# Optimization experiments

Hardware: AMD Instinct MI355X
Metric: run time of the kernel (lower is better)

The kernel has to match this reference:

```python
import jax, jax.numpy as jnp
import numpy as np

B, N, PHY, C, HID, FC, L, E = 2, 8192, 2, 64, 64, 128, 3, 524288

def _ln(x, g, b, eps=1e-5):
    mu = jnp.mean(x, axis=-1, keepdims=True)
    var = jnp.mean((x - mu) ** 2, axis=-1, keepdims=True)
    return (x - mu) * jax.lax.rsqrt(var + eps) * g + b

def setup_inputs() -> dict:
    key = jax.random.key(0)
    ks = jax.random.split(key, 24)
    s = 1.0 / np.sqrt(C)
    inp = {
        'x': jax.random.normal(ks[0], (B, N, 5), jnp.float32),
        'edge_index': jax.random.randint(ks[1], (2, E), 0, B * N, jnp.int32),
        'fc0_w': jax.random.normal(ks[2], (C, 4), jnp.float32) * 0.5,
        'fc0_b': jnp.zeros((C,), jnp.float32),
        'ln0_g': jnp.ones((C,), jnp.float32),
        'ln0_b': jnp.zeros((C,), jnp.float32),
        'gg_fc1_w': jax.random.normal(ks[3], (L, HID, C), jnp.float32) * s,
        'gg_fc1_b': jnp.zeros((L, HID), jnp.float32),
        'gg_fc2_w': jax.random.normal(ks[4], (L, C, HID), jnp.float32) * s,
        'gg_fc2_b': jnp.zeros((L, C), jnp.float32),
        'gg_weight': jax.random.uniform(ks[5], (L, HID), jnp.float32) + 0.5,
        'gg_freq': jax.random.normal(ks[6], (L, PHY, HID), jnp.float32) * (2 * np.pi),
        'wc_w': jax.random.normal(ks[7], (L, C, C), jnp.float32) * s,
        'wc_b': jnp.zeros((L, C), jnp.float32),
        'ln_g': jnp.ones((L, C), jnp.float32),
        'ln_b': jnp.zeros((L, C), jnp.float32),
        'fc1_w': jax.random.normal(ks[8], (FC, C), jnp.float32) * s,
        'fc1_b': jnp.zeros((FC,), jnp.float32),
        'fc2_w': jax.random.normal(ks[9], (1, FC), jnp.float32) / np.sqrt(FC),
        'fc2_b': jnp.zeros((1,), jnp.float32),
    }
    return inp

def reference(x, edge_index, fc0_w, fc0_b, ln0_g, ln0_b, gg_fc1_w, gg_fc1_b,
              gg_fc2_w, gg_fc2_b, gg_weight, gg_freq, wc_w, wc_b, ln_g, ln_b,
              fc1_w, fc1_b, fc2_w, fc2_b):
    grid = x[:, :, 2:4]           # (B,N,PHY): columns in_dim-phy_dim .. -1
    gw = x[:, :, 4]               # (B,N) grid_weight
    feat = x[:, :, :4]            # (B,N,in_dim)
    src, dst = edge_index[0], edge_index[1]
    grid_f = grid.reshape(-1, PHY)
    gw_f = gw.reshape(-1)
    vec = grid_f[src] - grid_f[dst]                      # (E,PHY)
    dist2 = jnp.sum(vec * vec, axis=-1, keepdims=True)   # (E,1)
    wgt_src = gw_f[src][:, None]                          # (E,1)

    h = feat @ fc0_w.T + fc0_b                            # (B,N,C)
    h = _ln(h, ln0_g, ln0_b)
    for l in range(L):
        w = gg_weight[l]                                  # (HID,)
        gauss = jnp.sqrt((w / jnp.pi) ** PHY) * jnp.exp(-w * dist2)  # (E,HID)
        fourier = jnp.sin(vec @ gg_freq[l])               # (E,HID)
        morlet = gauss * fourier
        hl = h @ gg_fc1_w[l].T + gg_fc1_b[l]              # (B,N,HID)
        val = morlet * hl.reshape(-1, HID)[src] * wgt_src # (E,HID)
        agg = jax.ops.segment_sum(val, dst, num_segments=B * N)
        x1 = agg.reshape(B, N, HID) @ gg_fc2_w[l].T + gg_fc2_b[l]
        x2 = h @ wc_w[l].T + wc_b[l]                      # pointwise Conv1d
        h = _ln(x1 + x2, ln_g[l], ln_b[l])
        if l != L - 1:
            h = jax.nn.gelu(h, approximate=False)
    h = jax.nn.gelu(h @ fc1_w.T + fc1_b, approximate=False)
    return h @ fc2_w.T + fc2_b                            # (B,N,1)
```

## Files before the change

### kernel.cpp

```cpp
#include <hip/hip_runtime.h>
#include <hip/hip_bf16.h>

#define M_NODES 16384
#define E_EDGES 524288
#define ASTR 68

typedef short short8 __attribute__((ext_vector_type(8)));
typedef float f32x4 __attribute__((ext_vector_type(4)));
typedef unsigned int uint4v __attribute__((ext_vector_type(4)));

static __device__ __forceinline__ float wredsum(float v) {
#pragma unroll
  for (int o = 32; o > 0; o >>= 1) v += __shfl_xor(v, o, 64);
  return v;
}

static __device__ __forceinline__ float gelu_exact(float x) {
  return 0.5f * x * (1.0f + erff(x * 0.70710678118654752440f));
}

static __device__ __forceinline__ unsigned int bsplit(float x) {
  unsigned int u = __float_as_uint(x);
  unsigned int hb = (u + 0x7FFFu + ((u >> 16) & 1u)) >> 16;
  float hf = __uint_as_float(hb << 16);
  float r = x - hf;
  unsigned int v = __float_as_uint(r);
  unsigned int lb = (v + 0x7FFFu + ((v >> 16) & 1u)) >> 16;
  return (hb & 0xFFFFu) | (lb << 16);
}

struct Frag { short8 hi, lo; };

static __device__ __forceinline__ Frag load_afrag(const unsigned int* a) {
  uint4v u0 = *(const uint4v*)a;
  uint4v u1 = *(const uint4v*)(a + 4);
  Frag f;
#pragma unroll
  for (int j = 0; j < 4; ++j) {
    f.hi[j]     = (short)(u0[j] & 0xFFFFu);
    f.lo[j]     = (short)(u0[j] >> 16);
    f.hi[j + 4] = (short)(u1[j] & 0xFFFFu);
    f.lo[j + 4] = (short)(u1[j] >> 16);
  }
  return f;
}

static __device__ __forceinline__ Frag load_bfrag(const float* __restrict__ w) {
  float4 w0 = *(const float4*)w;
  float4 w1 = *(const float4*)(w + 4);
  float v[8] = {w0.x, w0.y, w0.z, w0.w, w1.x, w1.y, w1.z, w1.w};
  Frag f;
#pragma unroll
  for (int j = 0; j < 8; ++j) {
    unsigned int p = bsplit(v[j]);
    f.hi[j] = (short)(p & 0xFFFFu);
    f.lo[j] = (short)(p >> 16);
  }
  return f;
}

static __device__ __forceinline__ f32x4 mfma3(const Frag& a, const Frag& b, f32x4 c) {
  c = __builtin_amdgcn_mfma_f32_16x16x32_bf16(a.hi, b.hi, c, 0, 0, 0);
  c = __builtin_amdgcn_mfma_f32_16x16x32_bf16(a.lo, b.hi, c, 0, 0, 0);
  c = __builtin_amdgcn_mfma_f32_16x16x32_bf16(a.hi, b.lo, c, 0, 0, 0);
  return c;
}

static __device__ __forceinline__ void gemm64(const unsigned int* Arow,
                                              const float* __restrict__ W,
                                              int c, int q, f32x4 acc[4]) {
  Frag a0 = load_afrag(Arow + 8 * q);
  Frag a1 = load_afrag(Arow + 32 + 8 * q);
#pragma unroll
  for (int t = 0; t < 4; ++t) {
    Frag b0 = load_bfrag(W + (16 * t + c) * 64 + 8 * q);
    Frag b1 = load_bfrag(W + (16 * t + c) * 64 + 32 + 8 * q);
    acc[t] = mfma3(a0, b0, acc[t]);
    acc[t] = mfma3(a1, b1, acc[t]);
  }
}

static __device__ __forceinline__ void store_d(float* __restrict__ O,
                                               const float* __restrict__ bias,
                                               int tilebase, int c, int q,
                                               const f32x4 acc[4]) {
#pragma unroll
  for (int t = 0; t < 4; ++t) {
    float bn = bias[16 * t + c];
#pragma unroll
    for (int r = 0; r < 4; ++r)
      O[(tilebase + 4 * q + r) * 64 + 16 * t + c] = acc[t][r] + bn;
  }
}

__global__ __launch_bounds__(256) void k_init(
    const float* __restrict__ x,
    const float* __restrict__ fc0_w, const float* __restrict__ fc0_b,
    const float* __restrict__ ln0_g, const float* __restrict__ ln0_b,
    const float* __restrict__ w1, const float* __restrict__ b1,
    const float* __restrict__ wc, const float* __restrict__ wcb,
    float2* __restrict__ grid2, float* __restrict__ gwf,
    float* __restrict__ hl, float* __restrict__ x2)
{
  __shared__ unsigned int A[64 * ASTR];
  const int tid = threadIdx.x;
  const int lane = tid & 63;
  const int w = tid >> 6;
  const int tilebase = blockIdx.x * 64 + w * 16;

  float fw0 = fc0_w[lane * 4 + 0], fw1 = fc0_w[lane * 4 + 1];
  float fw2v = fc0_w[lane * 4 + 2], fw3 = fc0_w[lane * 4 + 3];
  float fb = fc0_b[lane], g0 = ln0_g[lane], bb0 = ln0_b[lane];

  for (int i = 0; i < 16; ++i) {
    int node = tilebase + i;
    float xv0 = x[node * 5 + 0], xv1 = x[node * 5 + 1], xv2 = x[node * 5 + 2];
    float xv3 = x[node * 5 + 3], xv4 = x[node * 5 + 4];
    float acc = fb + xv0 * fw0 + xv1 * fw1 + xv2 * fw2v + xv3 * fw3;
    float mean = wredsum(acc) * (1.0f / 64.0f);
    float d = acc - mean;
    float var = wredsum(d * d) * (1.0f / 64.0f);
    float hv = d * rsqrtf(var + 1e-5f) * g0 + bb0;
    A[(w * 16 + i) * ASTR + lane] = bsplit(hv);
    if (lane == 0) { grid2[node] = make_float2(xv2, xv3); gwf[node] = xv4; }
  }
  __syncthreads();

  const int c = lane & 15, q = lane >> 4;
  const unsigned int* Arow = A + (w * 16 + c) * ASTR;

  f32x4 z = {0.f, 0.f, 0.f, 0.f};
  f32x4 acc1[4] = {z, z, z, z};
  gemm64(Arow, w1, c, q, acc1);
  store_d(hl, b1, tilebase, c, q, acc1);

  f32x4 acc2[4] = {z, z, z, z};
  gemm64(Arow, wc, c, q, acc2);
  store_d(x2, wcb, tilebase, c, q, acc2);
}

__global__ __launch_bounds__(256) void k_count(const int* __restrict__ ei, int* __restrict__ cnt)
{
  int e = blockIdx.x * 256 + threadIdx.x;
  if (e < E_EDGES) atomicAdd(&cnt[ei[E_EDGES + e]], 1);
}

__global__ __launch_bounds__(1024) void k_scan(const int* __restrict__ cnt,
                                               int* __restrict__ row_start,
                                               int* __restrict__ cursor)
{
  const int PER = M_NODES / 1024;
  const int t = threadIdx.x;
  const int base = t * PER;
  int local[PER];
  int s = 0;
#pragma unroll
  for (int k = 0; k < PER; ++k) { local[k] = cnt[base + k]; s += local[k]; }

  __shared__ int part[1024];
  part[t] = s;
  __syncthreads();
  for (int off = 1; off < 1024; off <<= 1) {
    int v = (t >= off) ? part[t - off] : 0;
    __syncthreads();
    part[t] += v;
    __syncthreads();
  }
  int run = part[t] - s;
#pragma unroll
  for (int k = 0; k < PER; ++k) {
    row_start[base + k] = run;
    cursor[base + k] = run;
    run += local[k];
  }
  if (t == 1023) row_start[M_NODES] = run;
}

__global__ __launch_bounds__(256) void k_scatter(
    const int* __restrict__ ei, const float2* __restrict__ grid2,
    const float* __restrict__ gwf, int* __restrict__ cursor,
    float4* __restrict__ rec)
{
  int e = blockIdx.x * 256 + threadIdx.x;
  if (e < E_EDGES) {
    int s = ei[e];
    int dd = ei[E_EDGES + e];
    int pos = atomicAdd(&cursor[dd], 1);
    float2 gs = grid2[s], gd = grid2[dd];
    rec[pos] = make_float4(gs.x - gd.x, gs.y - gd.y, gwf[s], __int_as_float(s));
  }
}

__global__ __launch_bounds__(256) void k_agg(
    const float4* __restrict__ rec, const int* __restrict__ row_start,
    const float* __restrict__ hl,
    const float* __restrict__ gw, const float* __restrict__ freq,
    float* __restrict__ agg)
{
  const int lane = threadIdx.x & 63;
  const int node = blockIdx.x * 4 + (threadIdx.x >> 6);

  const float w = gw[lane];
  const float nwl2 = -w * 1.44269504088896340736f;
  const float lc = log2f(w * 0.31830988618379067154f);
  const float f0s = freq[lane] * 0.15915494309189533577f;
  const float f1s = freq[64 + lane] * 0.15915494309189533577f;

  const int beg = row_start[node];
  const int end = row_start[node + 1];
  float acc = 0.0f;

  int i = beg;
  if (i < end) {
    float4 r = rec[i];
    float hlv = hl[__float_as_int(r.w) * 64 + lane];
    for (++i; i < end; ++i) {
      float4 rn = rec[i];
      float hn = hl[__float_as_int(rn.w) * 64 + lane];
      float dist2 = r.x * r.x + r.y * r.y;
      float gs = __builtin_amdgcn_exp2f(__builtin_fmaf(nwl2, dist2, lc));
      float rev = __builtin_fmaf(r.x, f0s, r.y * f1s);
      float fo = __builtin_amdgcn_sinf(__builtin_amdgcn_fractf(rev));
      acc = __builtin_fmaf(gs * fo * hlv, r.z, acc);
      r = rn; hlv = hn;
    }
    float dist2 = r.x * r.x + r.y * r.y;
    float gs = __builtin_amdgcn_exp2f(__builtin_fmaf(nwl2, dist2, lc));
    float rev = __builtin_fmaf(r.x, f0s, r.y * f1s);
    float fo = __builtin_amdgcn_sinf(__builtin_amdgcn_fractf(rev));
    acc = __builtin_fmaf(gs * fo * hlv, r.z, acc);
  }
  agg[node * 64 + lane] = acc;
}

__global__ __launch_bounds__(256) void k_post_mid(
    const float* __restrict__ agg,
    const float* __restrict__ w2, const float* __restrict__ b2,
    const float* __restrict__ lng, const float* __restrict__ lnb,
    const float* __restrict__ nw1, const float* __restrict__ nb1,
    const float* __restrict__ nwc, const float* __restrict__ nwcb,
    float* __restrict__ hl, float* __restrict__ x2)
{
  __shared__ unsigned int A[64 * ASTR];
  const int tid = threadIdx.x, lane = tid & 63, w = tid >> 6;
  const int tilebase = blockIdx.x * 64 + w * 16;
  const int c = lane & 15, q = lane >> 4;

  float x2v[4][4], lg[4], lb[4], vb[4];
#pragma unroll
  for (int t = 0; t < 4; ++t) {
    int n = 16 * t + c;
    lg[t] = lng[n]; lb[t] = lnb[n]; vb[t] = b2[n];
#pragma unroll
    for (int r = 0; r < 4; ++r)
      x2v[t][r] = x2[(tilebase + 4 * q + r) * 64 + n];
  }

  {
    int rr = lane >> 2, cc = (lane & 3) * 16;
    const float* src = agg + (tilebase + rr) * 64 + cc;
    unsigned int* dstp = A + (16 * w + rr) * ASTR + cc;
#pragma unroll
    for (int j4 = 0; j4 < 4; ++j4) {
      float4 v = *(const float4*)(src + 4 * j4);
      uint4v pv;
      pv[0] = bsplit(v.x); pv[1] = bsplit(v.y); pv[2] = bsplit(v.z); pv[3] = bsplit(v.w);
      *(uint4v*)(dstp + 4 * j4) = pv;
    }
  }
  __syncthreads();

  const unsigned int* Arow = A + (16 * w + c) * ASTR;
  f32x4 z = {0.f, 0.f, 0.f, 0.f};
  f32x4 acc[4] = {z, z, z, z};
  gemm64(Arow, w2, c, q, acc);

  float v[4][4];
#pragma unroll
  for (int t = 0; t < 4; ++t)
#pragma unroll
    for (int r = 0; r < 4; ++r)
      v[t][r] = acc[t][r] + vb[t] + x2v[t][r];

  float mean[4], var[4];
#pragma unroll
  for (int r = 0; r < 4; ++r) {
    float s = v[0][r] + v[1][r] + v[2][r] + v[3][r];
    s += __shfl_xor(s, 1, 64); s += __shfl_xor(s, 2, 64);
    s += __shfl_xor(s, 4, 64); s += __shfl_xor(s, 8, 64);
    mean[r] = s * (1.0f / 64.0f);
  }
#pragma unroll
  for (int r = 0; r < 4; ++r) {
    float s = 0.f;
#pragma unroll
    for (int t = 0; t < 4; ++t) { float d = v[t][r] - mean[r]; s += d * d; }
    s += __shfl_xor(s, 1, 64); s += __shfl_xor(s, 2, 64);
    s += __shfl_xor(s, 4, 64); s += __shfl_xor(s, 8, 64);
    var[r] = s * (1.0f / 64.0f);
  }
#pragma unroll
  for (int t = 0; t < 4; ++t)
#pragma unroll
    for (int r = 0; r < 4; ++r) {
      float d = v[t][r] - mean[r];
      float h = d * rsqrtf(var[r] + 1e-5f) * lg[t] + lb[t];
      v[t][r] = gelu_exact(h);
    }

#pragma unroll
  for (int t = 0; t < 4; ++t)
#pragma unroll
    for (int r = 0; r < 4; ++r)
      A[(16 * w + 4 * q + r) * ASTR + 16 * t + c] = bsplit(v[t][r]);

  f32x4 acch[4] = {z, z, z, z};
  gemm64(Arow, nw1, c, q, acch);
  store_d(hl, nb1, tilebase, c, q, acch);

  f32x4 accx[4] = {z, z, z, z};
  gemm64(Arow, nwc, c, q, accx);
  store_d(x2, nwcb, tilebase, c, q, accx);
}

__global__ __launch_bounds__(256) void k_post_last(
    const float* __restrict__ agg,
    const float* __restrict__ w2, const float* __restrict__ b2,
    const float* __restrict__ lng, const float* __restrict__ lnb,
    const float* __restrict__ x2,
    const float* __restrict__ fc1w, const float* __restrict__ fc1b,
    const float* __restrict__ fw2, const float* __restrict__ fb2,
    float* __restrict__ out)
{
  __shared__ unsigned int A[64 * ASTR];
  const int tid = threadIdx.x, lane = tid & 63, w = tid >> 6;
  const int tilebase = blockIdx.x * 64 + w * 16;
  const int c = lane & 15, q = lane >> 4;

  float x2v[4][4], lg[4], lb[4], vb[4];
#pragma unroll
  for (int t = 0; t < 4; ++t) {
    int n = 16 * t + c;
    lg[t] = lng[n]; lb[t] = lnb[n]; vb[t] = b2[n];
#pragma unroll
    for (int r = 0; r < 4; ++r)
      x2v[t][r] = x2[(tilebase + 4 * q + r) * 64 + n];
  }

  {
    int rr = lane >> 2, cc = (lane & 3) * 16;
    const float* src = agg + (tilebase + rr) * 64 + cc;
    unsigned int* dstp = A + (16 * w + rr) * ASTR + cc;
#pragma unroll
    for (int j4 = 0; j4 < 4; ++j4) {
      float4 v = *(const float4*)(src + 4 * j4);
      uint4v pv;
      pv[0] = bsplit(v.x); pv[1] = bsplit(v.y); pv[2] = bsplit(v.z); pv[3] = bsplit(v.w);
      *(uint4v*)(dstp + 4 * j4) = pv;
    }
  }
  __syncthreads();

  const unsigned int* Arow = A + (16 * w + c) * ASTR;
  f32x4 z = {0.f, 0.f, 0.f, 0.f};
  f32x4 acc[4] = {z, z, z, z};
  gemm64(Arow, w2, c, q, acc);

  float v[4][4];
#pragma unroll
  for (int t = 0; t < 4; ++t)
#pragma unroll
    for (int r = 0; r < 4; ++r)
      v[t][r] = acc[t][r] + vb[t] + x2v[t][r];

  float mean[4], var[4];
#pragma unroll
  for (int r = 0; r < 4; ++r) {
    float s = v[0][r] + v[1][r] + v[2][r] + v[3][r];
    s += __shfl_xor(s, 1, 64); s += __shfl_xor(s, 2, 64);
    s += __shfl_xor(s, 4, 64); s += __shfl_xor(s, 8, 64);
    mean[r] = s * (1.0f / 64.0f);
  }
#pragma unroll
  for (int r = 0; r < 4; ++r) {
    float s = 0.f;
#pragma unroll
    for (int t = 0; t < 4; ++t) { float d = v[t][r] - mean[r]; s += d * d; }
    s += __shfl_xor(s, 1, 64); s += __shfl_xor(s, 2, 64);
    s += __shfl_xor(s, 4, 64); s += __shfl_xor(s, 8, 64);
    var[r] = s * (1.0f / 64.0f);
  }
#pragma unroll
  for (int t = 0; t < 4; ++t)
#pragma unroll
    for (int r = 0; r < 4; ++r) {
      float d = v[t][r] - mean[r];
      v[t][r] = d * rsqrtf(var[r] + 1e-5f) * lg[t] + lb[t];
    }

#pragma unroll
  for (int t = 0; t < 4; ++t)
#pragma unroll
    for (int r = 0; r < 4; ++r)
      A[(16 * w + 4 * q + r) * ASTR + 16 * t + c] = bsplit(v[t][r]);

  Frag a0 = load_afrag(Arow + 8 * q);
  Frag a1 = load_afrag(Arow + 32 + 8 * q);
  float p[4] = {0.f, 0.f, 0.f, 0.f};
#pragma unroll
  for (int t8 = 0; t8 < 8; ++t8) {
    Frag b0 = load_bfrag(fc1w + (16 * t8 + c) * 64 + 8 * q);
    Frag b1 = load_bfrag(fc1w + (16 * t8 + c) * 64 + 32 + 8 * q);
    f32x4 a = z;
    a = mfma3(a0, b0, a);
    a = mfma3(a1, b1, a);
    float fbv = fc1b[16 * t8 + c];
    float fwv = fw2[16 * t8 + c];
#pragma unroll
    for (int r = 0; r < 4; ++r) p[r] += gelu_exact(a[r] + fbv) * fwv;
  }
#pragma unroll
  for (int r = 0; r < 4; ++r) {
    float s = p[r];
    s += __shfl_xor(s, 1, 64); s += __shfl_xor(s, 2, 64);
    s += __shfl_xor(s, 4, 64); s += __shfl_xor(s, 8, 64);
    p[r] = s;
  }
  if (c == 0) {
    float bb = fb2[0];
#pragma unroll
    for (int r = 0; r < 4; ++r) out[tilebase + 4 * q + r] = p[r] + bb;
  }
}

extern "C" void kernel_launch(void* const* d_in, const int* in_sizes, int n_in,
                              void* d_out, int out_size, void* d_ws, size_t ws_size,
                              hipStream_t stream) {
  const float* x     = (const float*)d_in[0];
  const int* ei      = (const int*)d_in[1];
  const float* fc0_w = (const float*)d_in[2];
  const float* fc0_b = (const float*)d_in[3];
  const float* ln0_g = (const float*)d_in[4];
  const float* ln0_b = (const float*)d_in[5];
  const float* gg_fc1_w = (const float*)d_in[6];
  const float* gg_fc1_b = (const float*)d_in[7];
  const float* gg_fc2_w = (const float*)d_in[8];
  const float* gg_fc2_b = (const float*)d_in[9];
  const float* gg_weight = (const float*)d_in[10];
  const float* gg_freq   = (const float*)d_in[11];
  const float* wc_w = (const float*)d_in[12];
  const float* wc_b = (const float*)d_in[13];
  const float* ln_g = (const float*)d_in[14];
  const float* ln_b = (const float*)d_in[15];
  const float* fc1_w = (const float*)d_in[16];
  const float* fc1_b = (const float*)d_in[17];
  const float* fc2_w = (const float*)d_in[18];
  const float* fc2_b = (const float*)d_in[19];

  char* ws = (char*)d_ws;
  size_t off = 0;
  auto alloc = [&](size_t bytes) -> void* {
    void* p = ws + off;
    off = (off + bytes + 255) & ~(size_t)255;
    return p;
  };
  float2* grid2   = (float2*)alloc((size_t)M_NODES * 8);
  float*  gwf     = (float*)alloc((size_t)M_NODES * 4);
  float*  hl      = (float*)alloc((size_t)M_NODES * 64 * 4);
  float*  agg     = (float*)alloc((size_t)M_NODES * 64 * 4);
  float*  x2      = (float*)alloc((size_t)M_NODES * 64 * 4);
  int*    cnt     = (int*)alloc((size_t)M_NODES * 4);
  int*    cursor  = (int*)alloc((size_t)M_NODES * 4);
  int*    row_st  = (int*)alloc((size_t)(M_NODES + 1) * 4);
  float4* rec     = (float4*)alloc((size_t)E_EDGES * 16);
  (void)ws_size; (void)in_sizes; (void)n_in; (void)out_size;

  hipMemsetAsync(cnt, 0, (size_t)M_NODES * 4, stream);

  k_init<<<M_NODES / 64, 256, 0, stream>>>(x, fc0_w, fc0_b, ln0_g, ln0_b,
                                           gg_fc1_w, gg_fc1_b, wc_w, wc_b,
                                           grid2, gwf, hl, x2);
  k_count<<<E_EDGES / 256, 256, 0, stream>>>(ei, cnt);
  k_scan<<<1, 1024, 0, stream>>>(cnt, row_st, cursor);
  k_scatter<<<E_EDGES / 256, 256, 0, stream>>>(ei, grid2, gwf, cursor, rec);

  for (int l = 0; l < 3; ++l) {
    k_agg<<<M_NODES / 4, 256, 0, stream>>>(rec, row_st, hl,
                                           gg_weight + l * 64, gg_freq + l * 128, agg);
    if (l < 2) {
      k_post_mid<<<M_NODES / 64, 256, 0, stream>>>(
          agg,
          gg_fc2_w + l * 4096, gg_fc2_b + l * 64,
          ln_g + l * 64, ln_b + l * 64,
          gg_fc1_w + (l + 1) * 4096, gg_fc1_b + (l + 1) * 64,
          wc_w + (l + 1) * 4096, wc_b + (l + 1) * 64,
          hl, x2);
    } else {
      k_post_last<<<M_NODES / 64, 256, 0, stream>>>(
          agg,
          gg_fc2_w + l * 4096, gg_fc2_b + l * 64,
          ln_g + l * 64, ln_b + l * 64,
          x2,
          fc1_w, fc1_b, fc2_w, fc2_b,
          (float*)d_out);
    }
  }
}
```

Before: 310.3 us.

## Split dense node GEMMs across waves by output column, 16 nodes per block

The node-wise dense kernels (init, post_mid, post_last) now process 16 nodes per block instead of 64. Each of the four waves computes a 16-column slice of the output rather than all 64 columns for its own 16 rows. Grids grow from 256 to 1024 blocks, which gives more parallelism across CUs and fewer registers per thread. The cost is that LayerNorm statistics need a cross-wave reduction through shared memory with extra barriers, and variance now uses the single-pass E[x^2]-mean^2 form, which is slightly less numerically stable.

Result: faster. 288.0 us (-7.2%).

```diff
diff --git a/kernel.cpp b/kernel.cpp
--- a/kernel.cpp
+++ b/kernel.cpp
@@ -66,31 +66,17 @@
   return c;
 }
 
-static __device__ __forceinline__ void gemm64(const unsigned int* Arow,
-                                              const float* __restrict__ W,
-                                              int c, int q, f32x4 acc[4]) {
-  Frag a0 = load_afrag(Arow + 8 * q);
-  Frag a1 = load_afrag(Arow + 32 + 8 * q);
-#pragma unroll
-  for (int t = 0; t < 4; ++t) {
-    Frag b0 = load_bfrag(W + (16 * t + c) * 64 + 8 * q);
-    Frag b1 = load_bfrag(W + (16 * t + c) * 64 + 32 + 8 * q);
-    acc[t] = mfma3(a0, b0, acc[t]);
-    acc[t] = mfma3(a1, b1, acc[t]);
-  }
-}
-
-static __device__ __forceinline__ void store_d(float* __restrict__ O,
-                                               const float* __restrict__ bias,
-                                               int tilebase, int c, int q,
-                                               const f32x4 acc[4]) {
-#pragma unroll
-  for (int t = 0; t < 4; ++t) {
-    float bn = bias[16 * t + c];
-#pragma unroll
-    for (int r = 0; r < 4; ++r)
-      O[(tilebase + 4 * q + r) * 64 + 16 * t + c] = acc[t][r] + bn;
-  }
+static __device__ __forceinline__ f32x4 gemm16(const unsigned int* __restrict__ A,
+                                               const float* __restrict__ W,
+                                               int n, int c, int q) {
+  Frag a0 = load_afrag(A + c * ASTR + 8 * q);
+  Frag a1 = load_afrag(A + c * ASTR + 32 + 8 * q);
+  Frag b0 = load_bfrag(W + n * 64 + 8 * q);
+  Frag b1 = load_bfrag(W + n * 64 + 32 + 8 * q);
+  f32x4 acc = {0.f, 0.f, 0.f, 0.f};
+  acc = mfma3(a0, b0, acc);
+  acc = mfma3(a1, b1, acc);
+  return acc;
 }
 
 __global__ __launch_bounds__(256) void k_init(
@@ -102,18 +88,17 @@
     float2* __restrict__ grid2, float* __restrict__ gwf,
     float* __restrict__ hl, float* __restrict__ x2)
 {
-  __shared__ unsigned int A[64 * ASTR];
-  const int tid = threadIdx.x;
-  const int lane = tid & 63;
-  const int w = tid >> 6;
-  const int tilebase = blockIdx.x * 64 + w * 16;
+  __shared__ unsigned int A[16 * ASTR];
+  const int tid = threadIdx.x, lane = tid & 63, w = tid >> 6;
+  const int tilebase = blockIdx.x * 16;
 
   float fw0 = fc0_w[lane * 4 + 0], fw1 = fc0_w[lane * 4 + 1];
   float fw2v = fc0_w[lane * 4 + 2], fw3 = fc0_w[lane * 4 + 3];
   float fb = fc0_b[lane], g0 = ln0_g[lane], bb0 = ln0_b[lane];
 
-  for (int i = 0; i < 16; ++i) {
-    int node = tilebase + i;
+#pragma unroll
+  for (int i = 0; i < 4; ++i) {
+    int node = tilebase + 4 * w + i;
     float xv0 = x[node * 5 + 0], xv1 = x[node * 5 + 1], xv2 = x[node * 5 + 2];
     float xv3 = x[node * 5 + 3], xv4 = x[node * 5 + 4];
     float acc = fb + xv0 * fw0 + xv1 * fw1 + xv2 * fw2v + xv3 * fw3;
@@ -121,22 +106,25 @@
     float d = acc - mean;
     float var = wredsum(d * d) * (1.0f / 64.0f);
     float hv = d * rsqrtf(var + 1e-5f) * g0 + bb0;
-    A[(w * 16 + i) * ASTR + lane] = bsplit(hv);
+    A[(4 * w + i) * ASTR + lane] = bsplit(hv);
     if (lane == 0) { grid2[node] = make_float2(xv2, xv3); gwf[node] = xv4; }
   }
   __syncthreads();
 
   const int c = lane & 15, q = lane >> 4;
-  const unsigned int* Arow = A + (w * 16 + c) * ASTR;
-
-  f32x4 z = {0.f, 0.f, 0.f, 0.f};
-  f32x4 acc1[4] = {z, z, z, z};
-  gemm64(Arow, w1, c, q, acc1);
-  store_d(hl, b1, tilebase, c, q, acc1);
-
-  f32x4 acc2[4] = {z, z, z, z};
-  gemm64(Arow, wc, c, q, acc2);
-  store_d(x2, wcb, tilebase, c, q, acc2);
+  const int n = 16 * w + c;
+
+  f32x4 a1v = gemm16(A, w1, n, c, q);
+  float b1v = b1[n];
+#pragma unroll
+  for (int r = 0; r < 4; ++r)
+    hl[(tilebase + 4 * q + r) * 64 + n] = a1v[r] + b1v;
+
+  f32x4 a2v = gemm16(A, wc, n, c, q);
+  float wcbv = wcb[n];
+#pragma unroll
+  for (int r = 0; r < 4; ++r)
+    x2[(tilebase + 4 * q + r) * 64 + n] = a2v[r] + wcbv;
 }
 
 __global__ __launch_bounds__(256) void k_count(const int* __restrict__ ei, int* __restrict__ cnt)
@@ -241,86 +229,71 @@
     const float* __restrict__ nwc, const float* __restrict__ nwcb,
     float* __restrict__ hl, float* __restrict__ x2)
 {
-  __shared__ unsigned int A[64 * ASTR];
+  __shared__ unsigned int A[16 * ASTR];
+  __shared__ float PS[4][16], PQ[4][16];
   const int tid = threadIdx.x, lane = tid & 63, w = tid >> 6;
-  const int tilebase = blockIdx.x * 64 + w * 16;
+  const int tilebase = blockIdx.x * 16;
   const int c = lane & 15, q = lane >> 4;
-
-  float x2v[4][4], lg[4], lb[4], vb[4];
-#pragma unroll
-  for (int t = 0; t < 4; ++t) {
-    int n = 16 * t + c;
-    lg[t] = lng[n]; lb[t] = lnb[n]; vb[t] = b2[n];
-#pragma unroll
-    for (int r = 0; r < 4; ++r)
-      x2v[t][r] = x2[(tilebase + 4 * q + r) * 64 + n];
-  }
+  const int n = 16 * w + c;
+
+  float x2v[4];
+#pragma unroll
+  for (int r = 0; r < 4; ++r)
+    x2v[r] = x2[(tilebase + 4 * q + r) * 64 + n];
+  float lg = lng[n], lb = lnb[n], vb = b2[n];
 
   {
-    int rr = lane >> 2, cc = (lane & 3) * 16;
-    const float* src = agg + (tilebase + rr) * 64 + cc;
-    unsigned int* dstp = A + (16 * w + rr) * ASTR + cc;
-#pragma unroll
-    for (int j4 = 0; j4 < 4; ++j4) {
-      float4 v = *(const float4*)(src + 4 * j4);
-      uint4v pv;
-      pv[0] = bsplit(v.x); pv[1] = bsplit(v.y); pv[2] = bsplit(v.z); pv[3] = bsplit(v.w);
-      *(uint4v*)(dstp + 4 * j4) = pv;
+    int i = tid * 4;
+    int row = i >> 6, col = i & 63;
+    float4 v = *(const float4*)(agg + tilebase * 64 + i);
+    uint4v pv;
+    pv[0] = bsplit(v.x); pv[1] = bsplit(v.y); pv[2] = bsplit(v.z); pv[3] = bsplit(v.w);
+    *(uint4v*)(A + row * ASTR + col) = pv;
+  }
+  __syncthreads();
+
+  f32x4 acc = gemm16(A, w2, n, c, q);
+
+  float S[4];
+#pragma unroll
+  for (int r = 0; r < 4; ++r) S[r] = acc[r] + vb + x2v[r];
+
+#pragma unroll
+  for (int r = 0; r < 4; ++r) {
+    float s1 = S[r], s2 = S[r] * S[r];
+#pragma unroll
+    for (int m = 1; m < 16; m <<= 1) {
+      s1 += __shfl_xor(s1, m, 64);
+      s2 += __shfl_xor(s2, m, 64);
     }
-  }
-  __syncthreads();
-
-  const unsigned int* Arow = A + (16 * w + c) * ASTR;
-  f32x4 z = {0.f, 0.f, 0.f, 0.f};
-  f32x4 acc[4] = {z, z, z, z};
-  gemm64(Arow, w2, c, q, acc);
-
-  float v[4][4];
-#pragma unroll
-  for (int t = 0; t < 4; ++t)
-#pragma unroll
-    for (int r = 0; r < 4; ++r)
-      v[t][r] = acc[t][r] + vb[t] + x2v[t][r];
-
-  float mean[4], var[4];
+    if (c == 0) { PS[w][4 * q + r] = s1; PQ[w][4 * q + r] = s2; }
+  }
+  __syncthreads();
+
 #pragma unroll
   for (int r = 0; r < 4; ++r) {
-    float s = v[0][r] + v[1][r] + v[2][r] + v[3][r];
-    s += __shfl_xor(s, 1, 64); s += __shfl_xor(s, 2, 64);
-    s += __shfl_xor(s, 4, 64); s += __shfl_xor(s, 8, 64);
-    mean[r] = s * (1.0f / 64.0f);
-  }
-#pragma unroll
-  for (int r = 0; r < 4; ++r) {
-    float s = 0.f;
-#pragma unroll
-    for (int t = 0; t < 4; ++t) { float d = v[t][r] - mean[r]; s += d * d; }
-    s += __shfl_xor(s, 1, 64); s += __shfl_xor(s, 2, 64);
-    s += __shfl_xor(s, 4, 64); s += __shfl_xor(s, 8, 64);
-    var[r] = s * (1.0f / 64.0f);
-  }
-#pragma unroll
-  for (int t = 0; t < 4; ++t)
-#pragma unroll
-    for (int r = 0; r < 4; ++r) {
-      float d = v[t][r] - mean[r];
-      float h = d * rsqrtf(var[r] + 1e-5f) * lg[t] + lb[t];
-      v[t][r] = gelu_exact(h);
-    }
-
-#pragma unroll
-  for (int t = 0; t < 4; ++t)
-#pragma unroll
-    for (int r = 0; r < 4; ++r)
-      A[(16 * w + 4 * q + r) * ASTR + 16 * t + c] = bsplit(v[t][r]);
-
-  f32x4 acch[4] = {z, z, z, z};
-  gemm64(Arow, nw1, c, q, acch);
-  store_d(hl, nb1, tilebase, c, q, acch);
-
-  f32x4 accx[4] = {z, z, z, z};
-  gemm64(Arow, nwc, c, q, accx);
-  store_d(x2, nwcb, tilebase, c, q, accx);
+    int row = 4 * q + r;
+    float sum = PS[0][row] + PS[1][row] + PS[2][row] + PS[3][row];
+    float sq  = PQ[0][row] + PQ[1][row] + PQ[2][row] + PQ[3][row];
+    float mean = sum * (1.0f / 64.0f);
+    float var = sq * (1.0f / 64.0f) - mean * mean;
+    float hv = (S[r] - mean) * rsqrtf(var + 1e-5f) * lg + lb;
+    hv = gelu_exact(hv);
+    A[row * ASTR + n] = bsplit(hv);
+  }
+  __syncthreads();
+
+  f32x4 a1v = gemm16(A, nw1, n, c, q);
+  float b1v = nb1[n];
+#pragma unroll
+  for (int r = 0; r < 4; ++r)
+    hl[(tilebase + 4 * q + r) * 64 + n] = a1v[r] + b1v;
+
+  f32x4 a2v = gemm16(A, nwc, n, c, q);
+  float wcbv = nwcb[n];
+#pragma unroll
+  for (int r = 0; r < 4; ++r)
+    x2[(tilebase + 4 * q + r) * 64 + n] = a2v[r] + wcbv;
 }
 
 __global__ __launch_bounds__(256) void k_post_last(
@@ -332,105 +305,84 @@
     const float* __restrict__ fw2, const float* __restrict__ fb2,
     float* __restrict__ out)
 {
-  __shared__ unsigned int A[64 * ASTR];
+  __shared__ unsigned int A[16 * ASTR];
+  __shared__ float PS[4][16], PQ[4][16];
   const int tid = threadIdx.x, lane = tid & 63, w = tid >> 6;
-  const int tilebase = blockIdx.x * 64 + w * 16;
+  const int tilebase = blockIdx.x * 16;
   const int c = lane & 15, q = lane >> 4;
-
-  float x2v[4][4], lg[4], lb[4], vb[4];
-#pragma unroll
-  for (int t = 0; t < 4; ++t) {
-    int n = 16 * t + c;
-    lg[t] = lng[n]; lb[t] = lnb[n]; vb[t] = b2[n];
-#pragma unroll
-    for (int r = 0; r < 4; ++r)
-      x2v[t][r] = x2[(tilebase + 4 * q + r) * 64 + n];
-  }
+  const int n = 16 * w + c;
+
+  float x2v[4];
+#pragma unroll
+  for (int r = 0; r < 4; ++r)
+    x2v[r] = x2[(tilebase + 4 * q + r) * 64 + n];
+  float lg = lng[n], lb = lnb[n], vb = b2[n];
 
   {
-    int rr = lane >> 2, cc = (lane & 3) * 16;
-    const float* src = agg + (tilebase + rr) * 64 + cc;
-    unsigned int* dstp = A + (16 * w + rr) * ASTR + cc;
-#pragma unroll
-    for (int j4 = 0; j4 < 4; ++j4) {
-      float4 v = *(const float4*)(src + 4 * j4);
-      uint4v pv;
-      pv[0] = bsplit(v.x); pv[1] = bsplit(v.y); pv[2] = bsplit(v.z); pv[3] = bsplit(v.w);
-      *(uint4v*)(dstp + 4 * j4) = pv;
+    int i = tid * 4;
+    int row = i >> 6, col = i & 63;
+    float4 v = *(const float4*)(agg + tilebase * 64 + i);
+    uint4v pv;
+    pv[0] = bsplit(v.x); pv[1] = bsplit(v.y); pv[2] = bsplit(v.z); pv[3] = bsplit(v.w);
+    *(uint4v*)(A + row * ASTR + col) = pv;
+  }
+  __syncthreads();
+
+  f32x4 acc = gemm16(A, w2, n, c, q);
+
+  float S[4];
+#pragma unroll
+  for (int r = 0; r < 4; ++r) S[r] = acc[r] + vb + x2v[r];
+
+#pragma unroll
+  for (int r = 0; r < 4; ++r) {
+    float s1 = S[r], s2 = S[r] * S[r];
+#pragma unroll
+    for (int m = 1; m < 16; m <<= 1) {
+      s1 += __shfl_xor(s1, m, 64);
+      s2 += __shfl_xor(s2, m, 64);
     }
-  }
-  __syncthreads();
-
-  const unsigned int* Arow = A + (16 * w + c) * ASTR;
-  f32x4 z = {0.f, 0.f, 0.f, 0.f};
-  f32x4 acc[4] = {z, z, z, z};
-  gemm64(Arow, w2, c, q, acc);
-
-  float v[4][4];
-#pragma unroll
-  for (int t = 0; t < 4; ++t)
-#pragma unroll
-    for (int r = 0; r < 4; ++r)
-      v[t][r] = acc[t][r] + vb[t] + x2v[t][r];
-
-  float mean[4], var[4];
+    if (c == 0) { PS[w][4 * q + r] = s1; PQ[w][4 * q + r] = s2; }
+  }
+  __syncthreads();
+
 #pragma unroll
   for (int r = 0; r < 4; ++r) {
-    float s = v[0][r] + v[1][r] + v[2][r] + v[3][r];
-    s += __shfl_xor(s, 1, 64); s += __shfl_xor(s, 2, 64);
-    s += __shfl_xor(s, 4, 64); s += __shfl_xor(s, 8, 64);
-    mean[r] = s * (1.0f / 64.0f);
-  }
-#pragma unroll
-  for (int r = 0; r < 4; ++r) {
-    float s = 0.f;
-#pragma unroll
-    for (int t = 0; t < 4; ++t) { float d = v[t][r] - mean[r]; s += d * d; }
-    s += __shfl_xor(s, 1, 64); s += __shfl_xor(s, 2, 64);
-    s += __shfl_xor(s, 4, 64); s += __shfl_xor(s, 8, 64);
-    var[r] = s * (1.0f / 64.0f);
-  }
-#pragma unroll
-  for (int t = 0; t < 4; ++t)
-#pragma unroll
-    for (int r = 0; r < 4; ++r) {
-      float d = v[t][r] - mean[r];
-      v[t][r] = d * rsqrtf(var[r] + 1e-5f) * lg[t] + lb[t];
-    }
-
-#pragma unroll
-  for (int t = 0; t < 4; ++t)
-#pragma unroll
-    for (int r = 0; r < 4; ++r)
-      A[(16 * w + 4 * q + r) * ASTR + 16 * t + c] = bsplit(v[t][r]);
-
-  Frag a0 = load_afrag(Arow + 8 * q);
-  Frag a1 = load_afrag(Arow + 32 + 8 * q);
+    int row = 4 * q + r;
+    float sum = PS[0][row] + PS[1][row] + PS[2][row] + PS[3][row];
+    float sq  = PQ[0][row] + PQ[1][row] + PQ[2][row] + PQ[3][row];
+    float mean = sum * (1.0f / 64.0f);
+    float var = sq * (1.0f / 64.0f) - mean * mean;
+    float hv = (S[r] - mean) * rsqrtf(var + 1e-5f) * lg + lb;
+    A[row * ASTR + n] = bsplit(hv);
+  }
+  __syncthreads();
+
+  Frag ha0 = load_afrag(A + c * ASTR + 8 * q);
+  Frag ha1 = load_afrag(A + c * ASTR + 32 + 8 * q);
   float p[4] = {0.f, 0.f, 0.f, 0.f};
 #pragma unroll
-  for (int t8 = 0; t8 < 8; ++t8) {
-    Frag b0 = load_bfrag(fc1w + (16 * t8 + c) * 64 + 8 * q);
-    Frag b1 = load_bfrag(fc1w + (16 * t8 + c) * 64 + 32 + 8 * q);
-    f32x4 a = z;
-    a = mfma3(a0, b0, a);
-    a = mfma3(a1, b1, a);
-    float fbv = fc1b[16 * t8 + c];
-    float fwv = fw2[16 * t8 + c];
+  for (int half = 0; half < 2; ++half) {
+    int row = 32 * w + 16 * half + c;
+    Frag b0 = load_bfrag(fc1w + row * 64 + 8 * q);
+    Frag b1 = load_bfrag(fc1w + row * 64 + 32 + 8 * q);
+    f32x4 a = {0.f, 0.f, 0.f, 0.f};
+    a = mfma3(ha0, b0, a);
+    a = mfma3(ha1, b1, a);
+    float fbv = fc1b[row], fwv = fw2[row];
 #pragma unroll
     for (int r = 0; r < 4; ++r) p[r] += gelu_exact(a[r] + fbv) * fwv;
   }
 #pragma unroll
   for (int r = 0; r < 4; ++r) {
     float s = p[r];
-    s += __shfl_xor(s, 1, 64); s += __shfl_xor(s, 2, 64);
-    s += __shfl_xor(s, 4, 64); s += __shfl_xor(s, 8, 64);
-    p[r] = s;
-  }
-  if (c == 0) {
-    float bb = fb2[0];
-#pragma unroll
-    for (int r = 0; r < 4; ++r) out[tilebase + 4 * q + r] = p[r] + bb;
-  }
+#pragma unroll
+    for (int m = 1; m < 16; m <<= 1) s += __shfl_xor(s, m, 64);
+    if (c == 0) PS[w][4 * q + r] = s;
+  }
+  __syncthreads();
+  if (tid < 16)
+    out[tilebase + tid] = PS[0][tid] + PS[1][tid] + PS[2][tid] + PS[3][tid] + fb2[0];
 }
 
 extern "C" void kernel_launch(void* const* d_in, const int* in_sizes, int n_in,
@@ -477,7 +429,7 @@
 
   hipMemsetAsync(cnt, 0, (size_t)M_NODES * 4, stream);
 
-  k_init<<<M_NODES / 64, 256, 0, stream>>>(x, fc0_w, fc0_b, ln0_g, ln0_b,
+  k_init<<<M_NODES / 16, 256, 0, stream>>>(x, fc0_w, fc0_b, ln0_g, ln0_b,
                                            gg_fc1_w, gg_fc1_b, wc_w, wc_b,
                                            grid2, gwf, hl, x2);
   k_count<<<E_EDGES / 256, 256, 0, stream>>>(ei, cnt);
@@ -488,7 +440,7 @@
     k_agg<<<M_NODES / 4, 256, 0, stream>>>(rec, row_st, hl,
                                            gg_weight + l * 64, gg_freq + l * 128, agg);
     if (l < 2) {
-      k_post_mid<<<M_NODES / 64, 256, 0, stream>>>(
+      k_post_mid<<<M_NODES / 16, 256, 0, stream>>>(
           agg,
           gg_fc2_w + l * 4096, gg_fc2_b + l * 64,
           ln_g + l * 64, ln_b + l * 64,
@@ -496,7 +448,7 @@
           wc_w + (l + 1) * 4096, wc_b + (l + 1) * 64,
           hl, x2);
     } else {
-      k_post_last<<<M_NODES / 64, 256, 0, stream>>>(
+      k_post_last<<<M_NODES / 16, 256, 0, stream>>>(
           agg,
           gg_fc2_w + l * 4096, gg_fc2_b + l * 64,
           ln_g + l * 64, ln_b + l * 64,
```
